# Optimization experiments

Measured on AMD Instinct MI355X. Metric: run time of the kernel, lower is better.

## Reference

```python
import jax, jax.numpy as jnp
import numpy as np

HEADS = 4
DIM_HEAD = 32


def setup_inputs() -> dict:
    key = jax.random.key(0)
    k1, k2, k3 = jax.random.split(key, 3)
    b, dim, h, w = 16, 256, 64, 64
    hidden = HEADS * DIM_HEAD  # 128
    x = jax.random.normal(k1, (b, dim, h, w), dtype=jnp.float32)
    # 1x1 convs are just channel matmuls; store kernels as 2D matrices.
    W_qkv = jax.random.normal(k2, (3 * hidden, dim), dtype=jnp.float32) * 0.02
    W_out = jax.random.normal(k3, (dim, hidden), dtype=jnp.float32) * 0.02
    b_out = jnp.zeros((dim,), dtype=jnp.float32)
    return {"x": x, "W_qkv": W_qkv, "W_out": W_out, "b_out": b_out}


def reference(x, W_qkv, W_out, b_out):
    b, c, h, w = x.shape
    n = h * w
    # 1x1 conv: (b, 3*hidden, h, w) -> view (b, 3, heads, dim_head, n)
    qkv = jnp.einsum('bchw,oc->bohw', x, W_qkv)
    qkv = qkv.reshape(b, 3, HEADS, DIM_HEAD, n)
    q, k, v = qkv[:, 0], qkv[:, 1], qkv[:, 2]  # each (b, heads, dim_head, n)
    k = jax.nn.softmax(k, axis=-1)
    # context: (b, heads, dim_head, dim_head)
    context = jnp.einsum('bhdn,bhen->bhde', k, v)
    # out: (b, heads, dim_head, n)
    out = jnp.einsum('bhde,bhen->bhdn', context, q)
    out = out.reshape(b, HEADS * DIM_HEAD, h, w)
    # to_out 1x1 conv with bias
    y = jnp.einsum('bchw,oc->bohw', out, W_out) + b_out[None, :, None, None]
    return y
```

## Files before the change

kernel.cpp:

```cpp
#include <hip/hip_runtime.h>

typedef __attribute__((ext_vector_type(8))) short short8;
typedef __attribute__((ext_vector_type(4))) float f32x4;
typedef unsigned short u16;
typedef unsigned int u32;


__device__ __forceinline__ u16 f2bf(float f) {
    u32 x = __float_as_uint(f);
    u32 r = (x + 0x7fffu + ((x >> 16) & 1u)) >> 16;
    return (u16)r;
}
__device__ __forceinline__ float bf2f(u16 h) {
    return __uint_as_float(((u32)h) << 16);
}

typedef __attribute__((address_space(1))) u32 as1_u32;
typedef __attribute__((address_space(3))) u32 as3_u32;
__device__ __forceinline__ void gload16(const void* g, void* l) {
    __builtin_amdgcn_global_load_lds((as1_u32*)g, (as3_u32*)l, 16, 0, 0);
}

__global__ __launch_bounds__(256) void k_convW(const float* __restrict__ W,
                                               u16* __restrict__ Wb) {
    int idx = blockIdx.x * 256 + threadIdx.x;
    float4 v = *reinterpret_cast<const float4*>(W + idx * 4);
    u32 w0 = (u32)f2bf(v.x) | ((u32)f2bf(v.y) << 16);
    u32 w1 = (u32)f2bf(v.z) | ((u32)f2bf(v.w) << 16);
    uint2 o = {w0, w1};
    *reinterpret_cast<uint2*>(Wb + idx * 4) = o;
}

__global__ __launch_bounds__(256) void k_transpose(const float* __restrict__ x,
                                                   u16* __restrict__ xT) {
    __shared__ alignas(16) u16 tile[64 * 72];
    int t = threadIdx.x;
    int n0 = blockIdx.x * 64, c0 = blockIdx.y * 64, b = blockIdx.z;
    int rr = t >> 4, nq = (t & 15) * 4;
#pragma unroll
    for (int i = 0; i < 4; i++) {
        int cl = i * 16 + rr;
        float4 v = *reinterpret_cast<const float4*>(x + ((size_t)(b * 256 + c0 + cl) * 4096 + n0 + nq));
        u32 w0 = (u32)f2bf(v.x) | ((u32)f2bf(v.y) << 16);
        u32 w1 = (u32)f2bf(v.z) | ((u32)f2bf(v.w) << 16);
        uint2 o = {w0, w1};
        *reinterpret_cast<uint2*>(&tile[cl * 72 + nq]) = o;
    }
    __syncthreads();
    int r = t >> 3, c8 = (t & 7) * 8;
#pragma unroll
    for (int i = 0; i < 2; i++) {
        int nl = i * 32 + r;
        alignas(16) u16 vals[8];
#pragma unroll
        for (int j = 0; j < 8; j++) vals[j] = tile[(c8 + j) * 72 + nl];
        *reinterpret_cast<uint4*>(xT + ((size_t)(b * 4096 + n0 + nl) * 256 + c0 + c8)) =
            *reinterpret_cast<const uint4*>(vals);
    }
}

__global__ __launch_bounds__(512, 4) void k_fused(const u16* __restrict__ xT,
                                                  const u16* __restrict__ Wb,
                                                  float* __restrict__ part,
                                                  float* __restrict__ denp) {
    __shared__ alignas(16) char smem[70656];
    u16* sA = (u16*)smem;
    u16* sB = (u16*)(smem + 32768);
    u16* Pl = (u16*)smem;
    u16* Vl = (u16*)(smem + 34816);
    float* dpart = (float*)(smem + 69632);

    int t = threadIdx.x;
    int nt = blockIdx.x, b = blockIdx.y;
    int n0 = nt * 128;
    int lane = t & 63, wv = t >> 6, l16 = lane & 15, lq = lane >> 4;
    int wr = wv >> 1, wc = wv & 1;
    int trow = t >> 3, tc8 = (t & 7) * 8;

    f32x4 acc[4][4];
#pragma unroll
    for (int i = 0; i < 4; i++)
#pragma unroll
        for (int j = 0; j < 4; j++) acc[i][j] = (f32x4){0.f, 0.f, 0.f, 0.f};

    const u16* Asrc = Wb + 128 * 256;
    const u16* Bsrc = xT + (size_t)(b * 4096 + n0) * 256;

    for (int kc = 0; kc < 4; kc++) {
        __syncthreads();
#pragma unroll
        for (int q = 0; q < 4; q++) {
            int row = q * 64 + trow;
            gload16(Asrc + (size_t)row * 256 + kc * 64 + tc8, &sA[row * 64 + tc8]);
        }
#pragma unroll
        for (int q = 0; q < 2; q++) {
            int row = q * 64 + trow;
            gload16(Bsrc + (size_t)row * 256 + kc * 64 + tc8, &sB[row * 64 + tc8]);
        }
        __syncthreads();
#pragma unroll
        for (int ks = 0; ks < 2; ks++) {
            int col = ks * 32 + lq * 8;
            short8 af[4], bfr[4];
#pragma unroll
            for (int i = 0; i < 4; i++)
                af[i] = *reinterpret_cast<const short8*>(&sA[(wr * 64 + i * 16 + l16) * 64 + col]);
#pragma unroll
            for (int j = 0; j < 4; j++)
                bfr[j] = *reinterpret_cast<const short8*>(&sB[(wc * 64 + j * 16 + l16) * 64 + col]);
#pragma unroll
            for (int i = 0; i < 4; i++)
#pragma unroll
                for (int j = 0; j < 4; j++)
                    acc[i][j] = __builtin_amdgcn_mfma_f32_16x16x32_bf16(af[i], bfr[j], acc[i][j], 0, 0, 0);
        }
    }
    __syncthreads();

    if (wr < 2) {
#pragma unroll
        for (int i = 0; i < 4; i++) {
            int rbase = wr * 64 + i * 16 + lq * 4;
            float srow[4] = {0.f, 0.f, 0.f, 0.f};
#pragma unroll
            for (int j = 0; j < 4; j++) {
                int n = wc * 64 + j * 16 + l16;
#pragma unroll
                for (int rr = 0; rr < 4; rr++) {
                    float e = __expf(acc[i][j][rr]);
                    Pl[(rbase + rr) * 136 + n] = f2bf(e);
                    srow[rr] += e;
                }
            }
#pragma unroll
            for (int rr = 0; rr < 4; rr++) {
                float s = srow[rr];
                s += __shfl_xor(s, 1, 64); s += __shfl_xor(s, 2, 64);
                s += __shfl_xor(s, 4, 64); s += __shfl_xor(s, 8, 64);
                if (l16 == 0) dpart[(rbase + rr) * 2 + wc] = s;
            }
        }
    } else {
#pragma unroll
        for (int i = 0; i < 4; i++) {
            int rbase = (wr - 2) * 64 + i * 16 + lq * 4;
#pragma unroll
            for (int j = 0; j < 4; j++) {
                int n = wc * 64 + j * 16 + l16;
#pragma unroll
                for (int rr = 0; rr < 4; rr++)
                    Vl[(rbase + rr) * 136 + n] = f2bf(acc[i][j][rr]);
            }
        }
    }
    __syncthreads();

    int h = wv >> 1, eh = wv & 1;
    f32x4 a2[2];
    a2[0] = (f32x4){0.f, 0.f, 0.f, 0.f};
    a2[1] = (f32x4){0.f, 0.f, 0.f, 0.f};
#pragma unroll
    for (int kk = 0; kk < 4; kk++) {
        int col = kk * 32 + lq * 8;
        short8 bfr = *reinterpret_cast<const short8*>(&Vl[(h * 32 + eh * 16 + l16) * 136 + col]);
#pragma unroll
        for (int i = 0; i < 2; i++) {
            short8 af = *reinterpret_cast<const short8*>(&Pl[(h * 32 + i * 16 + l16) * 136 + col]);
            a2[i] = __builtin_amdgcn_mfma_f32_16x16x32_bf16(af, bfr, a2[i], 0, 0, 0);
        }
    }
    float* pp = part + ((size_t)(b * 32 + nt) * 4 + h) * 1024;
#pragma unroll
    for (int i = 0; i < 2; i++)
#pragma unroll
        for (int rr = 0; rr < 4; rr++)
            pp[(i * 16 + lq * 4 + rr) * 32 + eh * 16 + l16] = a2[i][rr];

    if (t < 128)
        denp[((size_t)b * 128 + t) * 32 + nt] = dpart[t * 2] + dpart[t * 2 + 1];
}

__global__ __launch_bounds__(256) void k_red(const float* __restrict__ part,
                                             const float* __restrict__ denp,
                                             float* __restrict__ C) {
    __shared__ float invd[32];
    int bh = blockIdx.x;
    int b = bh >> 2, h = bh & 3;
    int t = threadIdx.x;
    if (t < 32) {
        const float* dp = denp + ((size_t)b * 128 + h * 32 + t) * 32;
        float s = 0.f;
#pragma unroll
        for (int nt = 0; nt < 32; nt++) s += dp[nt];
        invd[t] = 1.0f / s;
    }
    __syncthreads();
    int de0 = t * 4;
    float a0 = 0.f, a1 = 0.f, a2 = 0.f, a3 = 0.f;
#pragma unroll 8
    for (int nt = 0; nt < 32; nt++) {
        f32x4 v = *reinterpret_cast<const f32x4*>(part + ((size_t)(b * 32 + nt) * 4 + h) * 1024 + de0);
        a0 += v[0]; a1 += v[1]; a2 += v[2]; a3 += v[3];
    }
    float iv = invd[de0 >> 5];
    f32x4 o = {a0 * iv, a1 * iv, a2 * iv, a3 * iv};
    *reinterpret_cast<f32x4*>(C + (size_t)bh * 1024 + de0) = o;
}

__global__ __launch_bounds__(256) void k_G(const float* __restrict__ C,
                                           const float* __restrict__ Wout,
                                           const u16* __restrict__ Wb,
                                           u16* __restrict__ Gb) {
    __shared__ float Cs[4096];
    __shared__ float Us[2048];
    int b = blockIdx.x, ot = blockIdx.y, ch = blockIdx.z, t = threadIdx.x;
    int o0 = ot * 16;
#pragma unroll
    for (int q = 0; q < 16; q++) {
        int idx = q * 256 + t;
        Cs[idx] = C[(size_t)b * 4096 + idx];
    }
    __syncthreads();
#pragma unroll
    for (int q = 0; q < 8; q++) {
        int idx = q * 256 + t;
        int ol = idx >> 7, he = idx & 127;
        int h = he >> 5, e = he & 31;
        const float* wrow = Wout + (o0 + ol) * 128 + h * 32;
        const float* crow = &Cs[h * 1024 + e];
        float a = 0.f;
#pragma unroll
        for (int d = 0; d < 32; d++) a += wrow[d] * crow[d * 32];
        Us[idx] = a;
    }
    __syncthreads();
    int ol = t >> 4, c0 = ch * 128 + (t & 15) * 8;
    float acc[8];
#pragma unroll
    for (int cc = 0; cc < 8; cc++) acc[cc] = 0.f;
    const float* Ur = &Us[ol * 128];
#pragma unroll 4
    for (int he = 0; he < 128; he++) {
        float u = Ur[he];
        short8 w8 = *reinterpret_cast<const short8*>(Wb + he * 256 + c0);
#pragma unroll
        for (int e = 0; e < 8; e++)
            acc[e] += u * bf2f((u16)w8[e]);
    }
    alignas(16) u16 ob[8];
#pragma unroll
    for (int cc = 0; cc < 8; cc++) ob[cc] = f2bf(acc[cc]);
    *reinterpret_cast<uint4*>(Gb + (size_t)(b * 256 + o0 + ol) * 256 + c0) =
        *reinterpret_cast<const uint4*>(ob);
}

__global__ __launch_bounds__(256) void k_y(const u16* __restrict__ Gb,
                                           const u16* __restrict__ xT,
                                           const float* __restrict__ bout,
                                           float* __restrict__ y) {
    __shared__ alignas(16) u16 sA[128 * 64];
    __shared__ alignas(16) u16 sB[128 * 64];
    int t = threadIdx.x;
    int mt = blockIdx.x, n0 = blockIdx.y * 128, b = blockIdx.z;
    int m0 = mt * 128;
    int lane = t & 63, wv = t >> 6, l16 = lane & 15, lq = lane >> 4;
    int wr = wv >> 1, wc = wv & 1;
    int trow = t >> 3, tc8 = (t & 7) * 8;

    f32x4 acc[4][4];
#pragma unroll
    for (int i = 0; i < 4; i++)
#pragma unroll
        for (int j = 0; j < 4; j++) acc[i][j] = (f32x4){0.f, 0.f, 0.f, 0.f};

    const u16* Asrc = Gb + (size_t)(b * 256 + m0) * 256;
    const u16* Bsrc = xT + (size_t)(b * 4096 + n0) * 256;

    for (int kc = 0; kc < 4; kc++) {
        __syncthreads();
#pragma unroll
        for (int q = 0; q < 4; q++) {
            int row = q * 32 + trow;
            gload16(Asrc + (size_t)row * 256 + kc * 64 + tc8, &sA[row * 64 + tc8]);
            gload16(Bsrc + (size_t)row * 256 + kc * 64 + tc8, &sB[row * 64 + tc8]);
        }
        __syncthreads();
#pragma unroll
        for (int ks = 0; ks < 2; ks++) {
            int col = ks * 32 + lq * 8;
            short8 af[4], bfr[4];
#pragma unroll
            for (int i = 0; i < 4; i++)
                af[i] = *reinterpret_cast<const short8*>(&sA[(wr * 64 + i * 16 + l16) * 64 + col]);
#pragma unroll
            for (int j = 0; j < 4; j++)
                bfr[j] = *reinterpret_cast<const short8*>(&sB[(wc * 64 + j * 16 + l16) * 64 + col]);
#pragma unroll
            for (int i = 0; i < 4; i++)
#pragma unroll
                for (int j = 0; j < 4; j++)
                    acc[i][j] = __builtin_amdgcn_mfma_f32_16x16x32_bf16(af[i], bfr[j], acc[i][j], 0, 0, 0);
        }
    }
#pragma unroll
    for (int i = 0; i < 4; i++) {
        int obase = m0 + wr * 64 + i * 16 + lq * 4;
#pragma unroll
        for (int j = 0; j < 4; j++) {
            int n = n0 + wc * 64 + j * 16 + l16;
#pragma unroll
            for (int rr = 0; rr < 4; rr++) {
                int o = obase + rr;
                y[(size_t)(b * 256 + o) * 4096 + n] = acc[i][j][rr] + bout[o];
            }
        }
    }
}

extern "C" void kernel_launch(void* const* d_in, const int* in_sizes, int n_in,
                              void* d_out, int out_size, void* d_ws, size_t ws_size,
                              hipStream_t stream) {
    const float* x    = (const float*)d_in[0];
    const float* Wqkv = (const float*)d_in[1];
    const float* Wout = (const float*)d_in[2];
    const float* bout = (const float*)d_in[3];
    float* y = (float*)d_out;

    char* ws = (char*)d_ws;
    u16*   xT   = (u16*)(ws);
    float* part = (float*)(ws + 33554432);
    float* denp = (float*)(ws + 41943040);
    float* C    = (float*)(ws + 42205184);
    u16*   Gb   = (u16*)(ws + 42467328);
    u16*   Wb   = (u16*)(ws + 44564480);

    k_convW    <<<96, 256, 0, stream>>>(Wqkv, Wb);
    k_transpose<<<dim3(64, 4, 16), 256, 0, stream>>>(x, xT);
    k_fused    <<<dim3(32, 16), 512, 0, stream>>>(xT, Wb, part, denp);
    k_red      <<<64, 256, 0, stream>>>(part, denp, C);
    k_G        <<<dim3(16, 16, 2), 256, 0, stream>>>(C, Wout, Wb, Gb);
    k_y        <<<dim3(2, 32, 16), 256, 0, stream>>>(Gb, xT, bout, y);
}
```

Baseline: 175.0 us.

## Fold weight conversion into transpose kernel and widen k_y tile to all outputs

```diff
diff --git a/kernel.cpp b/kernel.cpp
--- a/kernel.cpp
+++ b/kernel.cpp
@@ -21,21 +21,24 @@
     __builtin_amdgcn_global_load_lds((as1_u32*)g, (as3_u32*)l, 16, 0, 0);
 }
 
-__global__ __launch_bounds__(256) void k_convW(const float* __restrict__ W,
-                                               u16* __restrict__ Wb) {
-    int idx = blockIdx.x * 256 + threadIdx.x;
-    float4 v = *reinterpret_cast<const float4*>(W + idx * 4);
-    u32 w0 = (u32)f2bf(v.x) | ((u32)f2bf(v.y) << 16);
-    u32 w1 = (u32)f2bf(v.z) | ((u32)f2bf(v.w) << 16);
-    uint2 o = {w0, w1};
-    *reinterpret_cast<uint2*>(Wb + idx * 4) = o;
-}
-
 __global__ __launch_bounds__(256) void k_transpose(const float* __restrict__ x,
-                                                   u16* __restrict__ xT) {
+                                                   u16* __restrict__ xT,
+                                                   const float* __restrict__ W,
+                                                   u16* __restrict__ Wb) {
     __shared__ alignas(16) u16 tile[64 * 72];
     int t = threadIdx.x;
     int n0 = blockIdx.x * 64, c0 = blockIdx.y * 64, b = blockIdx.z;
+
+    int flat = (b * 4 + blockIdx.y) * 64 + blockIdx.x;
+    if (flat < 96) {
+        int idx = flat * 256 + t;
+        float4 v = *reinterpret_cast<const float4*>(W + (size_t)idx * 4);
+        u32 w0 = (u32)f2bf(v.x) | ((u32)f2bf(v.y) << 16);
+        u32 w1 = (u32)f2bf(v.z) | ((u32)f2bf(v.w) << 16);
+        uint2 o = {w0, w1};
+        *reinterpret_cast<uint2*>(Wb + (size_t)idx * 4) = o;
+    }
+
     int rr = t >> 4, nq = (t & 15) * 4;
 #pragma unroll
     for (int i = 0; i < 4; i++) {
@@ -255,15 +258,15 @@
         *reinterpret_cast<const uint4*>(ob);
 }
 
-__global__ __launch_bounds__(256) void k_y(const u16* __restrict__ Gb,
-                                           const u16* __restrict__ xT,
-                                           const float* __restrict__ bout,
-                                           float* __restrict__ y) {
-    __shared__ alignas(16) u16 sA[128 * 64];
+__global__ __launch_bounds__(512, 4) void k_y(const u16* __restrict__ Gb,
+                                              const u16* __restrict__ xT,
+                                              const float* __restrict__ bout,
+                                              float* __restrict__ y) {
+    __shared__ alignas(16) u16 sA[256 * 64];
     __shared__ alignas(16) u16 sB[128 * 64];
     int t = threadIdx.x;
-    int mt = blockIdx.x, n0 = blockIdx.y * 128, b = blockIdx.z;
-    int m0 = mt * 128;
+    int nt = blockIdx.x, b = blockIdx.y;
+    int n0 = nt * 128;
     int lane = t & 63, wv = t >> 6, l16 = lane & 15, lq = lane >> 4;
     int wr = wv >> 1, wc = wv & 1;
     int trow = t >> 3, tc8 = (t & 7) * 8;
@@ -274,15 +277,19 @@
 #pragma unroll
         for (int j = 0; j < 4; j++) acc[i][j] = (f32x4){0.f, 0.f, 0.f, 0.f};
 
-    const u16* Asrc = Gb + (size_t)(b * 256 + m0) * 256;
+    const u16* Asrc = Gb + (size_t)b * 256 * 256;
     const u16* Bsrc = xT + (size_t)(b * 4096 + n0) * 256;
 
     for (int kc = 0; kc < 4; kc++) {
         __syncthreads();
 #pragma unroll
         for (int q = 0; q < 4; q++) {
-            int row = q * 32 + trow;
+            int row = q * 64 + trow;
             gload16(Asrc + (size_t)row * 256 + kc * 64 + tc8, &sA[row * 64 + tc8]);
+        }
+#pragma unroll
+        for (int q = 0; q < 2; q++) {
+            int row = q * 64 + trow;
             gload16(Bsrc + (size_t)row * 256 + kc * 64 + tc8, &sB[row * 64 + tc8]);
         }
         __syncthreads();
@@ -305,7 +312,7 @@
     }
 #pragma unroll
     for (int i = 0; i < 4; i++) {
-        int obase = m0 + wr * 64 + i * 16 + lq * 4;
+        int obase = wr * 64 + i * 16 + lq * 4;
 #pragma unroll
         for (int j = 0; j < 4; j++) {
             int n = n0 + wc * 64 + j * 16 + l16;
@@ -335,10 +342,9 @@
     u16*   Gb   = (u16*)(ws + 42467328);
     u16*   Wb   = (u16*)(ws + 44564480);
 
-    k_convW    <<<96, 256, 0, stream>>>(Wqkv, Wb);
-    k_transpose<<<dim3(64, 4, 16), 256, 0, stream>>>(x, xT);
+    k_transpose<<<dim3(64, 4, 16), 256, 0, stream>>>(x, xT, Wqkv, Wb);
     k_fused    <<<dim3(32, 16), 512, 0, stream>>>(xT, Wb, part, denp);
     k_red      <<<64, 256, 0, stream>>>(part, denp, C);
     k_G        <<<dim3(16, 16, 2), 256, 0, stream>>>(C, Wout, Wb, Gb);
-    k_y        <<<dim3(2, 32, 16), 256, 0, stream>>>(Gb, xT, bout, y);
-}
+    k_y        <<<dim3(32, 16), 512, 0, stream>>>(Gb, xT, bout, y);
+}
```

After: 171.4 us. 2.0% less time.
